# Kernel tuning notes

Hardware: AMD Instinct MI355X
Metric: run time of the kernel (lower is better)

## Reference

```python
import jax, jax.numpy as jnp
import numpy as np

ALPHA = 10.0  # anchor scale: anchors = eye(C) * ALPHA


def setup_inputs() -> dict:
    key = jax.random.key(0)
    k_x, k_w = jax.random.split(key)
    B, D, C = 16384, 768, 1024
    x = jax.random.normal(k_x, (B, D), dtype=jnp.float32)
    # nn.Linear(input_dim, num_classes, bias=False).weight has shape (C, D)
    W = jax.random.normal(k_w, (C, D), dtype=jnp.float32) * (1.0 / np.sqrt(D))
    return {"x": x, "W": W}


def reference(x, W):
    # logits: (B, C) = x @ W^T
    logits = jnp.einsum("bd,cd->bc", x, W)
    # distances[b, j] = || logits[b] - alpha * e_j ||_2
    # = sqrt(||logits[b]||^2 - 2*alpha*logits[b, j] + alpha^2)
    # (exact algebraic identity for diagonal anchors; avoids the (B, C, C) intermediate)
    sq_norm = jnp.sum(logits * logits, axis=-1, keepdims=True)  # (B, 1)
    d2 = sq_norm - 2.0 * ALPHA * logits + ALPHA * ALPHA          # (B, C)
    distances = jnp.sqrt(jnp.maximum(d2, 0.0))
    return logits, distances
```

## Files before the change

### kernel.cpp

```cpp
#include <hip/hip_runtime.h>
#include <hip/hip_bf16.h>
#include <stdint.h>


#define M_DIM 16384
#define N_DIM 1024
#define K_DIM 768
#define ALPHA_F 10.0f

typedef __bf16 bf16x8 __attribute__((ext_vector_type(8)));
typedef float f32x4 __attribute__((ext_vector_type(4)));
typedef const __attribute__((address_space(1))) void* gas_ptr;
typedef __attribute__((address_space(3))) void* las_ptr;

#define WAITV(N) asm volatile("s_waitcnt vmcnt(" #N ")" ::: "memory")

static __device__ __forceinline__ void bar() {
  asm volatile("" ::: "memory");
  __builtin_amdgcn_s_barrier();
  asm volatile("" ::: "memory");
}

__global__ __launch_bounds__(256) void cvt_both_kernel(const float* __restrict__ x,
                                                       const float* __restrict__ Wm,
                                                       unsigned short* __restrict__ xb,
                                                       unsigned short* __restrict__ Wb) {
  const int nx4 = M_DIM * K_DIM / 4;
  const int nw4 = N_DIM * K_DIM / 4;
  int stride = gridDim.x * blockDim.x;
  for (int i = blockIdx.x * blockDim.x + threadIdx.x; i < nx4 + nw4; i += stride) {
    const float4* src;
    ushort4* dst;
    int j;
    if (i < nx4) { src = (const float4*)x; dst = (ushort4*)xb; j = i; }
    else { src = (const float4*)Wm; dst = (ushort4*)Wb; j = i - nx4; }
    float4 v = src[j];
    union { __bf16 h[4]; ushort4 u; } p;
    p.h[0] = (__bf16)v.x; p.h[1] = (__bf16)v.y;
    p.h[2] = (__bf16)v.z; p.h[3] = (__bf16)v.w;
    dst[j] = p.u;
  }
}

template <int MI0, int NI0>
__device__ __forceinline__ void mfma_quad(f32x4 (&acc)[8][4], bf16x8 (&af)[8][2],
                                          bf16x8 (&bq)[4][2]) {
#pragma unroll
  for (int mi = 0; mi < 4; ++mi)
#pragma unroll
    for (int ni = 0; ni < 2; ++ni)
#pragma unroll
      for (int kk = 0; kk < 2; ++kk)
        acc[MI0 + mi][NI0 + ni] = __builtin_amdgcn_mfma_f32_16x16x32_bf16(
            af[MI0 + mi][kk], bq[NI0 + ni][kk], acc[MI0 + mi][NI0 + ni], 0, 0, 0);
}

__global__ __launch_bounds__(512, 2) void gemm_bf16_kernel(
    const unsigned short* __restrict__ A,
    const unsigned short* __restrict__ B,
    float* __restrict__ C) {
  __shared__ __align__(16) unsigned short lds[2][4][128 * 64];

  const int t = threadIdx.x;
  const int lane = t & 63;
  const int w = t >> 6;
  const int wr = w >> 2;
  const int wc = w & 3;

  int bid = blockIdx.x;
  int swz = (bid & 7) * 32 + (bid >> 3);
  int tn = swz & 3;
  int tm = swz >> 2;

  const unsigned short* Abase = A + (size_t)tm * 256 * K_DIM;
  const unsigned short* Bbase = B + (size_t)tn * 256 * K_DIM;

  const int s0 = t;
  const int s1 = t + 512;
  const int r0 = s0 >> 3, c0 = s0 & 7;
  const int r1 = s1 >> 3, c1 = s1 & 7;

  auto stage = [&](int buf, int hf, int kt) {
    const unsigned short* gb =
        (hf < 2 ? Abase : Bbase) + (size_t)((hf & 1) * 128) * K_DIM + kt * 64;
    unsigned short* lb = &lds[buf][hf][0];
    {
      int cs = c0 ^ (r0 & 7);
      __builtin_amdgcn_global_load_lds((gas_ptr)(gb + (size_t)r0 * K_DIM + cs * 8),
                                       (las_ptr)(lb + s0 * 8), 16, 0, 0);
    }
    {
      int cs = c1 ^ (r1 & 7);
      __builtin_amdgcn_global_load_lds((gas_ptr)(gb + (size_t)r1 * K_DIM + cs * 8),
                                       (las_ptr)(lb + s1 * 8), 16, 0, 0);
    }
  };

  f32x4 acc[8][4] = {};
  bf16x8 af[8][2];
  bf16x8 bq[4][2];

  auto ld_a = [&](int buf, int mi, int kk) -> bf16x8 {
    int row = mi * 16 + (lane & 15);
    int cs = (kk * 4 + (lane >> 4)) ^ (row & 7);
    return *(const bf16x8*)(&lds[buf][wr][0] + row * 64 + cs * 8);
  };
  auto ld_b = [&](int buf, int ni, int kk) -> bf16x8 {
    int row = (wc & 1) * 64 + ni * 16 + (lane & 15);
    int cs = (kk * 4 + (lane >> 4)) ^ (row & 7);
    return *(const bf16x8*)(&lds[buf][2 + (wc >> 1)][0] + row * 64 + cs * 8);
  };

  auto loadA = [&](int buf, int m0) {
#pragma unroll
    for (int mi = 0; mi < 4; ++mi) {
      af[m0 + mi][0] = ld_a(buf, m0 + mi, 0);
      af[m0 + mi][1] = ld_a(buf, m0 + mi, 1);
    }
  };
  auto loadB = [&](int buf, int n0) {
#pragma unroll
    for (int ni = 0; ni < 2; ++ni) {
      bq[n0 + ni][0] = ld_b(buf, n0 + ni, 0);
      bq[n0 + ni][1] = ld_b(buf, n0 + ni, 1);
    }
  };

  stage(0, 0, 0); stage(0, 1, 0); stage(0, 2, 0); stage(0, 3, 0);
  stage(1, 0, 1); stage(1, 1, 1);
  WAITV(4);
  bar();

#pragma unroll 1
  for (int i = 0; i < 5; ++i) {
    const int kt0 = 2 * i, kt1 = 2 * i + 1;
    loadA(0, 0); loadB(0, 0);
    stage(1, 2, kt1);
    bar();
    __builtin_amdgcn_s_setprio(1); mfma_quad<0, 0>(acc, af, bq); __builtin_amdgcn_s_setprio(0);
    bar();
    loadA(0, 4);
    stage(1, 3, kt1);
    bar();
    __builtin_amdgcn_s_setprio(1); mfma_quad<4, 0>(acc, af, bq); __builtin_amdgcn_s_setprio(0);
    bar();
    loadB(0, 2);
    stage(0, 0, kt0 + 2);
    bar();
    __builtin_amdgcn_s_setprio(1); mfma_quad<0, 2>(acc, af, bq); __builtin_amdgcn_s_setprio(0);
    bar();
    stage(0, 1, kt0 + 2);
    bar();
    __builtin_amdgcn_s_setprio(1); mfma_quad<4, 2>(acc, af, bq); __builtin_amdgcn_s_setprio(0);
    WAITV(4);
    bar();
    loadA(1, 0); loadB(1, 0);
    stage(0, 2, kt0 + 2);
    bar();
    __builtin_amdgcn_s_setprio(1); mfma_quad<0, 0>(acc, af, bq); __builtin_amdgcn_s_setprio(0);
    bar();
    loadA(1, 4);
    stage(0, 3, kt0 + 2);
    bar();
    __builtin_amdgcn_s_setprio(1); mfma_quad<4, 0>(acc, af, bq); __builtin_amdgcn_s_setprio(0);
    bar();
    loadB(1, 2);
    stage(1, 0, kt1 + 2);
    bar();
    __builtin_amdgcn_s_setprio(1); mfma_quad<0, 2>(acc, af, bq); __builtin_amdgcn_s_setprio(0);
    bar();
    stage(1, 1, kt1 + 2);
    bar();
    __builtin_amdgcn_s_setprio(1); mfma_quad<4, 2>(acc, af, bq); __builtin_amdgcn_s_setprio(0);
    WAITV(4);
    bar();
  }

  loadA(0, 0); loadB(0, 0);
  stage(1, 2, 11);
  bar();
  __builtin_amdgcn_s_setprio(1); mfma_quad<0, 0>(acc, af, bq); __builtin_amdgcn_s_setprio(0);
  bar();
  loadA(0, 4);
  stage(1, 3, 11);
  bar();
  __builtin_amdgcn_s_setprio(1); mfma_quad<4, 0>(acc, af, bq); __builtin_amdgcn_s_setprio(0);
  bar();
  loadB(0, 2);
  bar();
  __builtin_amdgcn_s_setprio(1); mfma_quad<0, 2>(acc, af, bq); __builtin_amdgcn_s_setprio(0);
  bar();
  __builtin_amdgcn_s_setprio(1); mfma_quad<4, 2>(acc, af, bq); __builtin_amdgcn_s_setprio(0);
  WAITV(0);
  bar();
  loadA(1, 0); loadB(1, 0);
  loadA(1, 4); loadB(1, 2);
  __builtin_amdgcn_s_setprio(1);
  mfma_quad<0, 0>(acc, af, bq);
  mfma_quad<4, 0>(acc, af, bq);
  mfma_quad<0, 2>(acc, af, bq);
  mfma_quad<4, 2>(acc, af, bq);
  __builtin_amdgcn_s_setprio(0);

  float* Cb = C + ((size_t)tm * 256 + wr * 128) * N_DIM + tn * 256 + wc * 64;
#pragma unroll
  for (int mi = 0; mi < 8; ++mi)
#pragma unroll
    for (int ni = 0; ni < 4; ++ni) {
      int col = ni * 16 + (lane & 15);
      int row0 = mi * 16 + ((lane >> 4) << 2);
      f32x4 v = acc[mi][ni];
#pragma unroll
      for (int r = 0; r < 4; ++r)
        Cb[(size_t)(row0 + r) * N_DIM + col] = v[r];
    }
}

__global__ __launch_bounds__(256) void dist_kernel(const float* __restrict__ logits,
                                                   float* __restrict__ dist) {
  __shared__ float wsum[4];
  const int row = blockIdx.x;
  const int t = threadIdx.x;
  const float4* lr = reinterpret_cast<const float4*>(logits + (size_t)row * N_DIM);
  float4 v = lr[t];
  float ss = v.x * v.x + v.y * v.y + v.z * v.z + v.w * v.w;
#pragma unroll
  for (int m = 32; m >= 1; m >>= 1) ss += __shfl_xor(ss, m, 64);
  if ((t & 63) == 0) wsum[t >> 6] = ss;
  __syncthreads();
  float sq = wsum[0] + wsum[1] + wsum[2] + wsum[3];
  const float a2 = ALPHA_F * ALPHA_F;
  float4 d;
  d.x = sqrtf(fmaxf(sq - 2.0f * ALPHA_F * v.x + a2, 0.0f));
  d.y = sqrtf(fmaxf(sq - 2.0f * ALPHA_F * v.y + a2, 0.0f));
  d.z = sqrtf(fmaxf(sq - 2.0f * ALPHA_F * v.z + a2, 0.0f));
  d.w = sqrtf(fmaxf(sq - 2.0f * ALPHA_F * v.w + a2, 0.0f));
  reinterpret_cast<float4*>(dist + (size_t)row * N_DIM)[t] = d;
}

extern "C" void kernel_launch(void* const* d_in, const int* in_sizes, int n_in,
                              void* d_out, int out_size, void* d_ws, size_t ws_size,
                              hipStream_t stream) {
  const float* x = (const float*)d_in[0];
  const float* W = (const float*)d_in[1];
  float* logits = (float*)d_out;
  float* dist = logits + (size_t)M_DIM * N_DIM;

  unsigned short* xb = (unsigned short*)d_ws;
  unsigned short* Wb = xb + (size_t)M_DIM * K_DIM;

  cvt_both_kernel<<<2048, 256, 0, stream>>>(x, W, xb, Wb);
  gemm_bf16_kernel<<<(M_DIM / 256) * (N_DIM / 256), 512, 0, stream>>>(xb, Wb, logits);
  dist_kernel<<<M_DIM, 256, 0, stream>>>(logits, dist);
}
```

Measured before the change: 68.57 us.

## Fuse fp32-to-bf16 conversion of x into GEMM A-tile staging

The GEMM now loads x directly as fp32 into registers, converts it to bf16 and writes it into swizzled LDS, so the separate conversion pass over x and its workspace round trip go away. Only W is still converted by a small kernel. The main loop is rebuilt as a single-k-step double-buffered pipeline with register prefetch two steps ahead and explicit lgkm/vm waits. The dist kernel also visits rows in a reversed, interleaved order so it reads recently written logits while they may still be cached. In exchange the GEMM moves twice the A bytes from global memory, holds more registers, and waits on vmcnt(0) every step.

```diff
diff --git a/kernel.cpp b/kernel.cpp
--- a/kernel.cpp
+++ b/kernel.cpp
@@ -14,6 +14,9 @@
 typedef __attribute__((address_space(3))) void* las_ptr;
 
 #define WAITV(N) asm volatile("s_waitcnt vmcnt(" #N ")" ::: "memory")
+#define LGKM0 asm volatile("s_waitcnt lgkmcnt(0)" ::: "memory")
+#define PRIO1 __builtin_amdgcn_s_setprio(1)
+#define PRIO0 __builtin_amdgcn_s_setprio(0)
 
 static __device__ __forceinline__ void bar() {
   asm volatile("" ::: "memory");
@@ -21,25 +24,14 @@
   asm volatile("" ::: "memory");
 }
 
-__global__ __launch_bounds__(256) void cvt_both_kernel(const float* __restrict__ x,
-                                                       const float* __restrict__ Wm,
-                                                       unsigned short* __restrict__ xb,
-                                                       unsigned short* __restrict__ Wb) {
-  const int nx4 = M_DIM * K_DIM / 4;
-  const int nw4 = N_DIM * K_DIM / 4;
-  int stride = gridDim.x * blockDim.x;
-  for (int i = blockIdx.x * blockDim.x + threadIdx.x; i < nx4 + nw4; i += stride) {
-    const float4* src;
-    ushort4* dst;
-    int j;
-    if (i < nx4) { src = (const float4*)x; dst = (ushort4*)xb; j = i; }
-    else { src = (const float4*)Wm; dst = (ushort4*)Wb; j = i - nx4; }
-    float4 v = src[j];
-    union { __bf16 h[4]; ushort4 u; } p;
-    p.h[0] = (__bf16)v.x; p.h[1] = (__bf16)v.y;
-    p.h[2] = (__bf16)v.z; p.h[3] = (__bf16)v.w;
-    dst[j] = p.u;
-  }
+__global__ __launch_bounds__(256) void cvt_w_kernel(const float* __restrict__ in,
+                                                    unsigned short* __restrict__ out) {
+  int i = blockIdx.x * 256 + threadIdx.x;
+  f32x4 v = reinterpret_cast<const f32x4*>(in)[i];
+  union { __bf16 h[4]; ushort4 u; } p;
+  p.h[0] = (__bf16)v[0]; p.h[1] = (__bf16)v[1];
+  p.h[2] = (__bf16)v[2]; p.h[3] = (__bf16)v[3];
+  reinterpret_cast<ushort4*>(out)[i] = p.u;
 }
 
 template <int MI0, int NI0>
@@ -55,8 +47,8 @@
             af[MI0 + mi][kk], bq[NI0 + ni][kk], acc[MI0 + mi][NI0 + ni], 0, 0, 0);
 }
 
-__global__ __launch_bounds__(512, 2) void gemm_bf16_kernel(
-    const unsigned short* __restrict__ A,
+__global__ __launch_bounds__(512, 2) void gemm_fused_kernel(
+    const float* __restrict__ X,
     const unsigned short* __restrict__ B,
     float* __restrict__ C) {
   __shared__ __align__(16) unsigned short lds[2][4][128 * 64];
@@ -72,28 +64,50 @@
   int tn = swz & 3;
   int tm = swz >> 2;
 
-  const unsigned short* Abase = A + (size_t)tm * 256 * K_DIM;
+  const float* Xbase = X + (size_t)tm * 256 * K_DIM;
   const unsigned short* Bbase = B + (size_t)tn * 256 * K_DIM;
 
-  const int s0 = t;
-  const int s1 = t + 512;
+  const int s0 = t, s1 = t + 512;
   const int r0 = s0 >> 3, c0 = s0 & 7;
   const int r1 = s1 >> 3, c1 = s1 & 7;
-
-  auto stage = [&](int buf, int hf, int kt) {
-    const unsigned short* gb =
-        (hf < 2 ? Abase : Bbase) + (size_t)((hf & 1) * 128) * K_DIM + kt * 64;
-    unsigned short* lb = &lds[buf][hf][0];
-    {
-      int cs = c0 ^ (r0 & 7);
-      __builtin_amdgcn_global_load_lds((gas_ptr)(gb + (size_t)r0 * K_DIM + cs * 8),
-                                       (las_ptr)(lb + s0 * 8), 16, 0, 0);
-    }
-    {
-      int cs = c1 ^ (r1 & 7);
-      __builtin_amdgcn_global_load_lds((gas_ptr)(gb + (size_t)r1 * K_DIM + cs * 8),
-                                       (las_ptr)(lb + s1 * 8), 16, 0, 0);
-    }
+  const int cc0 = c0 ^ (r0 & 7);
+  const int cc1 = c1 ^ (r1 & 7);
+
+  auto stageB = [&](int buf, int hf, int kt) {
+    const unsigned short* gb = Bbase + (size_t)(hf * 128) * K_DIM + kt * 64;
+    unsigned short* lb = &lds[buf][2 + hf][0];
+    __builtin_amdgcn_global_load_lds((gas_ptr)(gb + (size_t)r0 * K_DIM + cc0 * 8),
+                                     (las_ptr)(lb + s0 * 8), 16, 0, 0);
+    __builtin_amdgcn_global_load_lds((gas_ptr)(gb + (size_t)r1 * K_DIM + cc1 * 8),
+                                     (las_ptr)(lb + s1 * 8), 16, 0, 0);
+  };
+
+  f32x4 ar[8];
+  auto issueA = [&](int kt) {
+    const float* g0 = Xbase + (size_t)r0 * K_DIM + kt * 64 + cc0 * 8;
+    const float* g1 = Xbase + (size_t)r1 * K_DIM + kt * 64 + cc1 * 8;
+    const float* g2 = Xbase + (size_t)(128 + r0) * K_DIM + kt * 64 + cc0 * 8;
+    const float* g3 = Xbase + (size_t)(128 + r1) * K_DIM + kt * 64 + cc1 * 8;
+    ar[0] = ((const f32x4*)g0)[0]; ar[1] = ((const f32x4*)g0)[1];
+    ar[2] = ((const f32x4*)g1)[0]; ar[3] = ((const f32x4*)g1)[1];
+    ar[4] = ((const f32x4*)g2)[0]; ar[5] = ((const f32x4*)g2)[1];
+    ar[6] = ((const f32x4*)g3)[0]; ar[7] = ((const f32x4*)g3)[1];
+  };
+  auto cvt8 = [&](f32x4 a, f32x4 b) -> bf16x8 {
+    union { __bf16 h[8]; bf16x8 v; } p;
+    p.h[0] = (__bf16)a[0]; p.h[1] = (__bf16)a[1];
+    p.h[2] = (__bf16)a[2]; p.h[3] = (__bf16)a[3];
+    p.h[4] = (__bf16)b[0]; p.h[5] = (__bf16)b[1];
+    p.h[6] = (__bf16)b[2]; p.h[7] = (__bf16)b[3];
+    return p.v;
+  };
+  auto writeA0 = [&](int buf) {
+    *(bf16x8*)(&lds[buf][0][0] + s0 * 8) = cvt8(ar[0], ar[1]);
+    *(bf16x8*)(&lds[buf][0][0] + s1 * 8) = cvt8(ar[2], ar[3]);
+  };
+  auto writeA1 = [&](int buf) {
+    *(bf16x8*)(&lds[buf][1][0] + s0 * 8) = cvt8(ar[4], ar[5]);
+    *(bf16x8*)(&lds[buf][1][0] + s1 * 8) = cvt8(ar[6], ar[7]);
   };
 
   f32x4 acc[8][4] = {};
@@ -110,7 +124,6 @@
     int cs = (kk * 4 + (lane >> 4)) ^ (row & 7);
     return *(const bf16x8*)(&lds[buf][2 + (wc >> 1)][0] + row * 64 + cs * 8);
   };
-
   auto loadA = [&](int buf, int m0) {
 #pragma unroll
     for (int mi = 0; mi < 4; ++mi) {
@@ -126,81 +139,54 @@
     }
   };
 
-  stage(0, 0, 0); stage(0, 1, 0); stage(0, 2, 0); stage(0, 3, 0);
-  stage(1, 0, 1); stage(1, 1, 1);
-  WAITV(4);
+  issueA(0);
+  stageB(0, 0, 0); stageB(0, 1, 0);
+  writeA0(0); writeA1(0);
+  issueA(1);
+  writeA0(1); writeA1(1);
+  LGKM0;
+  WAITV(0);
   bar();
 
 #pragma unroll 1
-  for (int i = 0; i < 5; ++i) {
-    const int kt0 = 2 * i, kt1 = 2 * i + 1;
-    loadA(0, 0); loadB(0, 0);
-    stage(1, 2, kt1);
-    bar();
-    __builtin_amdgcn_s_setprio(1); mfma_quad<0, 0>(acc, af, bq); __builtin_amdgcn_s_setprio(0);
-    bar();
-    loadA(0, 4);
-    stage(1, 3, kt1);
-    bar();
-    __builtin_amdgcn_s_setprio(1); mfma_quad<4, 0>(acc, af, bq); __builtin_amdgcn_s_setprio(0);
-    bar();
-    loadB(0, 2);
-    stage(0, 0, kt0 + 2);
-    bar();
-    __builtin_amdgcn_s_setprio(1); mfma_quad<0, 2>(acc, af, bq); __builtin_amdgcn_s_setprio(0);
-    bar();
-    stage(0, 1, kt0 + 2);
-    bar();
-    __builtin_amdgcn_s_setprio(1); mfma_quad<4, 2>(acc, af, bq); __builtin_amdgcn_s_setprio(0);
-    WAITV(4);
-    bar();
-    loadA(1, 0); loadB(1, 0);
-    stage(0, 2, kt0 + 2);
-    bar();
-    __builtin_amdgcn_s_setprio(1); mfma_quad<0, 0>(acc, af, bq); __builtin_amdgcn_s_setprio(0);
-    bar();
-    loadA(1, 4);
-    stage(0, 3, kt0 + 2);
-    bar();
-    __builtin_amdgcn_s_setprio(1); mfma_quad<4, 0>(acc, af, bq); __builtin_amdgcn_s_setprio(0);
-    bar();
-    loadB(1, 2);
-    stage(1, 0, kt1 + 2);
-    bar();
-    __builtin_amdgcn_s_setprio(1); mfma_quad<0, 2>(acc, af, bq); __builtin_amdgcn_s_setprio(0);
-    bar();
-    stage(1, 1, kt1 + 2);
-    bar();
-    __builtin_amdgcn_s_setprio(1); mfma_quad<4, 2>(acc, af, bq); __builtin_amdgcn_s_setprio(0);
-    WAITV(4);
-    bar();
+  for (int kt = 0; kt < 10; ++kt) {
+    const int buf = kt & 1, nbuf = buf ^ 1;
+    issueA(kt + 2);
+    stageB(nbuf, 0, kt + 1);
+    loadA(buf, 0); loadB(buf, 0);
+    bar(); PRIO1; mfma_quad<0, 0>(acc, af, bq); PRIO0; bar();
+    stageB(nbuf, 1, kt + 1);
+    loadA(buf, 4);
+    bar(); PRIO1; mfma_quad<4, 0>(acc, af, bq); PRIO0; bar();
+    loadB(buf, 2);
+    writeA0(buf);
+    LGKM0;
+    bar(); PRIO1; mfma_quad<0, 2>(acc, af, bq); PRIO0; bar();
+    writeA1(buf);
+    LGKM0;
+    WAITV(0);
+    bar(); PRIO1; mfma_quad<4, 2>(acc, af, bq); PRIO0; bar();
   }
 
+  stageB(1, 0, 11);
   loadA(0, 0); loadB(0, 0);
-  stage(1, 2, 11);
-  bar();
-  __builtin_amdgcn_s_setprio(1); mfma_quad<0, 0>(acc, af, bq); __builtin_amdgcn_s_setprio(0);
-  bar();
+  bar(); PRIO1; mfma_quad<0, 0>(acc, af, bq); PRIO0; bar();
+  stageB(1, 1, 11);
   loadA(0, 4);
-  stage(1, 3, 11);
-  bar();
-  __builtin_amdgcn_s_setprio(1); mfma_quad<4, 0>(acc, af, bq); __builtin_amdgcn_s_setprio(0);
-  bar();
+  bar(); PRIO1; mfma_quad<4, 0>(acc, af, bq); PRIO0; bar();
   loadB(0, 2);
-  bar();
-  __builtin_amdgcn_s_setprio(1); mfma_quad<0, 2>(acc, af, bq); __builtin_amdgcn_s_setprio(0);
-  bar();
-  __builtin_amdgcn_s_setprio(1); mfma_quad<4, 2>(acc, af, bq); __builtin_amdgcn_s_setprio(0);
+  bar(); PRIO1; mfma_quad<0, 2>(acc, af, bq); PRIO0; bar();
   WAITV(0);
+  bar(); PRIO1; mfma_quad<4, 2>(acc, af, bq); PRIO0;
   bar();
   loadA(1, 0); loadB(1, 0);
   loadA(1, 4); loadB(1, 2);
-  __builtin_amdgcn_s_setprio(1);
+  PRIO1;
   mfma_quad<0, 0>(acc, af, bq);
   mfma_quad<4, 0>(acc, af, bq);
   mfma_quad<0, 2>(acc, af, bq);
   mfma_quad<4, 2>(acc, af, bq);
-  __builtin_amdgcn_s_setprio(0);
+  PRIO0;
 
   float* Cb = C + ((size_t)tm * 256 + wr * 128) * N_DIM + tn * 256 + wc * 64;
 #pragma unroll
@@ -219,23 +205,23 @@
 __global__ __launch_bounds__(256) void dist_kernel(const float* __restrict__ logits,
                                                    float* __restrict__ dist) {
   __shared__ float wsum[4];
-  const int row = blockIdx.x;
+  const int bid = blockIdx.x;
+  const int row = (bid & 7) * 2048 + (2047 - (bid >> 3));
   const int t = threadIdx.x;
-  const float4* lr = reinterpret_cast<const float4*>(logits + (size_t)row * N_DIM);
-  float4 v = lr[t];
-  float ss = v.x * v.x + v.y * v.y + v.z * v.z + v.w * v.w;
+  const f32x4* lr = reinterpret_cast<const f32x4*>(logits + (size_t)row * N_DIM);
+  f32x4 v = lr[t];
+  float ss = v[0] * v[0] + v[1] * v[1] + v[2] * v[2] + v[3] * v[3];
 #pragma unroll
   for (int m = 32; m >= 1; m >>= 1) ss += __shfl_xor(ss, m, 64);
   if ((t & 63) == 0) wsum[t >> 6] = ss;
   __syncthreads();
   float sq = wsum[0] + wsum[1] + wsum[2] + wsum[3];
   const float a2 = ALPHA_F * ALPHA_F;
-  float4 d;
-  d.x = sqrtf(fmaxf(sq - 2.0f * ALPHA_F * v.x + a2, 0.0f));
-  d.y = sqrtf(fmaxf(sq - 2.0f * ALPHA_F * v.y + a2, 0.0f));
-  d.z = sqrtf(fmaxf(sq - 2.0f * ALPHA_F * v.z + a2, 0.0f));
-  d.w = sqrtf(fmaxf(sq - 2.0f * ALPHA_F * v.w + a2, 0.0f));
-  reinterpret_cast<float4*>(dist + (size_t)row * N_DIM)[t] = d;
+  f32x4 d;
+#pragma unroll
+  for (int j = 0; j < 4; ++j)
+    d[j] = sqrtf(fmaxf(sq - 2.0f * ALPHA_F * v[j] + a2, 0.0f));
+  reinterpret_cast<f32x4*>(dist + (size_t)row * N_DIM)[t] = d;
 }
 
 extern "C" void kernel_launch(void* const* d_in, const int* in_sizes, int n_in,
@@ -246,10 +232,9 @@
   float* logits = (float*)d_out;
   float* dist = logits + (size_t)M_DIM * N_DIM;
 
-  unsigned short* xb = (unsigned short*)d_ws;
-  unsigned short* Wb = xb + (size_t)M_DIM * K_DIM;
-
-  cvt_both_kernel<<<2048, 256, 0, stream>>>(x, W, xb, Wb);
-  gemm_bf16_kernel<<<(M_DIM / 256) * (N_DIM / 256), 512, 0, stream>>>(xb, Wb, logits);
+  unsigned short* Wb = (unsigned short*)d_ws;
+
+  cvt_w_kernel<<<N_DIM * K_DIM / 4 / 256, 256, 0, stream>>>(W, Wb);
+  gemm_fused_kernel<<<(M_DIM / 256) * (N_DIM / 256), 512, 0, stream>>>(x, Wb, logits);
   dist_kernel<<<M_DIM, 256, 0, stream>>>(logits, dist);
 }
```

Result: slower. 79.91 us (+16.5%).
